# Kernel optimization log

Measured on AMD Instinct MI355X. Metric: run time of the kernel, lower is better.

The kernel has to match this reference:

```python
import jax, jax.numpy as jnp
import numpy as np

L_F, HOP, DELTA, L_S, COND, GH = 32, 16, 3, 96, 32, 64
B, T = 128, 48000


def setup_inputs() -> dict:
    key = jax.random.key(0)
    ks = jax.random.split(key, 12)
    s = 0.05
    return {
        "x": jax.random.normal(ks[0], (B, T), jnp.float32),
        # GRU (PyTorch layout): weight_ih (3H, L_S), weight_hh (3H, H)
        "W_ih": jax.random.normal(ks[1], (3 * GH, L_S), jnp.float32) * s,
        "W_hh": jax.random.normal(ks[2], (3 * GH, GH), jnp.float32) * s,
        "b_ih": jax.random.normal(ks[3], (3 * GH,), jnp.float32) * s,
        "b_hh": jax.random.normal(ks[4], (3 * GH,), jnp.float32) * s,
        # SlowBranch output projection -> cond_dim
        "W_cs": jax.random.normal(ks[5], (COND, GH), jnp.float32) * s,
        "b_cs": jax.random.normal(ks[6], (COND,), jnp.float32) * s,
        # FastEC MLP
        "W1": jax.random.normal(ks[7], (GH, L_F + COND), jnp.float32) * s,
        "b1": jax.random.normal(ks[8], (GH,), jnp.float32) * s,
        "W2": jax.random.normal(ks[9], (L_F, GH), jnp.float32) * s,
        "b2": jax.random.normal(ks[10], (L_F,), jnp.float32) * s,
    }


def reference(x, W_ih, W_hh, b_ih, b_hh, W_cs, b_cs, W1, b1, W2, b2):
    Bsz, Tlen = x.shape
    Nf = (Tlen - L_F) // HOP + 1
    win_s = DELTA * HOP * 2
    hop_s = DELTA * HOP
    Ns = (Tlen - win_s) // hop_s + 1

    f_starts = jnp.arange(Nf) * HOP                      # (Nf,)
    fast_idx = f_starts[:, None] + jnp.arange(L_F)       # (Nf, L_F)
    fast_frames = x[:, fast_idx]                         # (B, Nf, L_F)

    s_starts = jnp.arange(Ns) * hop_s
    slow_frames = x[:, s_starts[:, None] + jnp.arange(win_s)]  # (B, Ns, L_S)

    # Single-layer GRU over slow frames (PyTorch gate order r, z, n)
    def step(h, xt):
        gi = xt @ W_ih.T + b_ih                          # (B, 3H)
        gh = h @ W_hh.T + b_hh
        i_r, i_z, i_n = jnp.split(gi, 3, axis=-1)
        h_r, h_z, h_n = jnp.split(gh, 3, axis=-1)
        r = jax.nn.sigmoid(i_r + h_r)
        z = jax.nn.sigmoid(i_z + h_z)
        n = jnp.tanh(i_n + r * h_n)
        hn = (1.0 - z) * n + z * h
        return hn, hn

    h0 = jnp.zeros((Bsz, GH), x.dtype)
    _, hs = jax.lax.scan(step, h0, jnp.swapaxes(slow_frames, 0, 1))
    hs = jnp.swapaxes(hs, 0, 1)                          # (B, Ns, GH)
    c_s = hs @ W_cs.T + b_cs                             # (B, Ns, COND)

    # per-fast-frame conditioning vector (gather)
    idx = jnp.clip(jnp.arange(Nf) // DELTA - 1, 0, None)
    c = c_s[:, idx]                                      # (B, Nf, COND)

    # FastEC batched over all frames at once
    h = jnp.concatenate([fast_frames, c], axis=-1)       # (B, Nf, L_F+COND)
    h = jax.nn.relu(h @ W1.T + b1)
    y = h @ W2.T + b2                                    # (B, Nf, L_F)

    # overlap-add scatter
    out = jnp.zeros_like(x).at[:, fast_idx].add(y)
    return out
```

## Files before the change

kernel.cpp:

```cpp
#include <hip/hip_runtime.h>

constexpr int Bn  = 128;
constexpr int Tn  = 48000;
constexpr int NFn = 2999;
constexpr int NSn = 999;
constexpr int G3n = 192;
constexpr int GHn = 64;

typedef float f2 __attribute__((ext_vector_type(2)));

__global__ __launch_bounds__(192) void gi_kernel(const float* __restrict__ x,
                                                 const float* __restrict__ W_ih,
                                                 const float* __restrict__ b_ih,
                                                 float* __restrict__ GI) {
  __shared__ __align__(16) float WT[48 * 196];
  __shared__ float xs[1584];
  const int tile = blockIdx.x;
  const int b    = blockIdx.y;
  const int t0   = tile * 32;
  const int nt   = min(32, NSn - t0);
  const int tid  = threadIdx.x;

  const int span = (nt - 1) * 48 + 96;
  for (int i = tid; i < 1584; i += 192)
    xs[i] = (i < span) ? x[(size_t)b * Tn + t0 * 48 + i] : 0.0f;

  const int jq = tid % 48;
  const int tg = tid / 48;
  const int j0 = jq * 4;

  float acc[8][4];
#pragma unroll
  for (int u = 0; u < 8; ++u)
#pragma unroll
    for (int jj = 0; jj < 4; ++jj) acc[u][jj] = b_ih[j0 + jj];

  for (int half = 0; half < 2; ++half) {
    __syncthreads();
    for (int e = tid; e < 192 * 48; e += 192) {
      int j = e / 48, k = e % 48;
      WT[k * 196 + j] = W_ih[j * 96 + half * 48 + k];
    }
    __syncthreads();
    for (int k = 0; k < 48; ++k) {
      float4 w = *(const float4*)&WT[k * 196 + j0];
#pragma unroll
      for (int u = 0; u < 8; ++u) {
        float xv = xs[(tg * 8 + u) * 48 + half * 48 + k];
        acc[u][0] = fmaf(xv, w.x, acc[u][0]);
        acc[u][1] = fmaf(xv, w.y, acc[u][1]);
        acc[u][2] = fmaf(xv, w.z, acc[u][2]);
        acc[u][3] = fmaf(xv, w.w, acc[u][3]);
      }
    }
  }

#pragma unroll
  for (int u = 0; u < 8; ++u) {
    int tl = tg * 8 + u;
    if (tl < nt) {
      float4 st = make_float4(acc[u][0], acc[u][1], acc[u][2], acc[u][3]);
      *(float4*)&GI[(size_t)(b * NSn + t0 + tl) * G3n + j0] = st;
    }
  }
}

__device__ __forceinline__ float fsigmoid(float v) {
  return __fdividef(1.0f, 1.0f + __expf(-v));
}
__device__ __forceinline__ float ftanh_f(float v) {
  return 1.0f - __fdividef(2.0f, __expf(2.0f * v) + 1.0f);
}

__global__ __launch_bounds__(64, 1) void gru_kernel(const float* __restrict__ GI,
                                                    const float* __restrict__ W_hh,
                                                    const float* __restrict__ b_hh,
                                                    float* __restrict__ hs) {
  __shared__ __align__(16) float hbuf[64];
  const int b = blockIdx.x;
  const int j = threadIdx.x;

  f2 wr2[32], wz2[32], wn2[32];
  const f2* Wr = (const f2*)(W_hh + (size_t)j * 64);
  const f2* Wz = (const f2*)(W_hh + (size_t)(j + 64) * 64);
  const f2* Wn = (const f2*)(W_hh + (size_t)(j + 128) * 64);
#pragma unroll
  for (int q = 0; q < 32; ++q) { wr2[q] = Wr[q]; wz2[q] = Wz[q]; wn2[q] = Wn[q]; }
  const float br = b_hh[j], bz = b_hh[j + 64], bn = b_hh[j + 128];

  hbuf[j] = 0.0f;
  float hj = 0.0f;
  __syncthreads();

  const float* gp = GI + (size_t)b * NSn * G3n;
  float* hsp = hs + (size_t)b * NSn * GHn;

  float pr[3], pz[3], pn[3];
#pragma unroll
  for (int u = 0; u < 2; ++u) {
    pr[u] = gp[(size_t)u * G3n + j];
    pz[u] = gp[(size_t)u * G3n + 64 + j];
    pn[u] = gp[(size_t)u * G3n + 128 + j];
  }

  for (int t = 0; t < NSn; ++t) {
    const size_t off = (size_t)min(t + 2, NSn - 1) * G3n;
    pr[2] = gp[off + j];
    pz[2] = gp[off + 64 + j];
    pn[2] = gp[off + 128 + j];

    const f2* h2 = (const f2*)hbuf;
    f2 ar0 = {0.f, 0.f}, ar1 = {0.f, 0.f}, ar2 = {0.f, 0.f}, ar3 = {0.f, 0.f};
    f2 az0 = {0.f, 0.f}, az1 = {0.f, 0.f}, az2 = {0.f, 0.f}, az3 = {0.f, 0.f};
    f2 an0 = {0.f, 0.f}, an1 = {0.f, 0.f}, an2 = {0.f, 0.f}, an3 = {0.f, 0.f};
#pragma unroll
    for (int q = 0; q < 8; ++q) {
      f2 h0 = h2[q * 4 + 0], h1 = h2[q * 4 + 1], h2v = h2[q * 4 + 2], h3 = h2[q * 4 + 3];
      ar0 += wr2[q * 4 + 0] * h0; ar1 += wr2[q * 4 + 1] * h1;
      ar2 += wr2[q * 4 + 2] * h2v; ar3 += wr2[q * 4 + 3] * h3;
      az0 += wz2[q * 4 + 0] * h0; az1 += wz2[q * 4 + 1] * h1;
      az2 += wz2[q * 4 + 2] * h2v; az3 += wz2[q * 4 + 3] * h3;
      an0 += wn2[q * 4 + 0] * h0; an1 += wn2[q * 4 + 1] * h1;
      an2 += wn2[q * 4 + 2] * h2v; an3 += wn2[q * 4 + 3] * h3;
    }
    f2 sr = (ar0 + ar1) + (ar2 + ar3);
    f2 sz = (az0 + az1) + (az2 + az3);
    f2 sn = (an0 + an1) + (an2 + an3);

    float r = fsigmoid(pr[0] + br + sr.x + sr.y);
    float z = fsigmoid(pz[0] + bz + sz.x + sz.y);
    float n = ftanh_f(fmaf(r, bn + sn.x + sn.y, pn[0]));
    float hn = fmaf(z, hj - n, n);

    hbuf[j] = hn;
    hj = hn;
    hsp[(size_t)t * GHn + j] = hn;
    __syncthreads();

    pr[0] = pr[1]; pr[1] = pr[2];
    pz[0] = pz[1]; pz[1] = pz[2];
    pn[0] = pn[1]; pn[1] = pn[2];
  }
}

__global__ __launch_bounds__(256) void cs_kernel(const float* __restrict__ hs,
                                                 const float* __restrict__ W_cs,
                                                 const float* __restrict__ b_cs,
                                                 float* __restrict__ cs) {
  __shared__ __align__(16) float WcT[64 * 36];
  __shared__ __align__(16) float hsl[32 * 65];
  __shared__ __align__(16) float bcs[32];
  const int tile = blockIdx.x;
  const int b    = blockIdx.y;
  const int t0   = tile * 32;
  const int nt   = min(32, NSn - t0);
  const int tid  = threadIdx.x;

  for (int e = tid; e < 32 * 64; e += 256) {
    int i = e >> 6, k = e & 63;
    WcT[k * 36 + i] = W_cs[e];
  }
  for (int e = tid; e < nt * 64; e += 256) {
    int t = e >> 6, k = e & 63;
    hsl[t * 65 + k] = hs[((size_t)b * NSn + t0 + t) * GHn + k];
  }
  if (tid < 32) bcs[tid] = b_cs[tid];
  __syncthreads();

  const int oq = tid & 7;
  const int t  = tid >> 3;
  if (t < nt) {
    float4 acc = *(const float4*)&bcs[oq * 4];
    const float* hr = &hsl[t * 65];
#pragma unroll 4
    for (int k = 0; k < 64; ++k) {
      float hv = hr[k];
      float4 w = *(const float4*)&WcT[k * 36 + oq * 4];
      acc.x = fmaf(w.x, hv, acc.x);
      acc.y = fmaf(w.y, hv, acc.y);
      acc.z = fmaf(w.z, hv, acc.z);
      acc.w = fmaf(w.w, hv, acc.w);
    }
    *(float4*)&cs[((size_t)b * NSn + t0 + t) * 32 + oq * 4] = acc;
  }
}

__global__ __launch_bounds__(256) void out_kernel(const float* __restrict__ x,
                                                  const float* __restrict__ cs,
                                                  const float* __restrict__ W1,
                                                  const float* __restrict__ b1,
                                                  const float* __restrict__ W2,
                                                  const float* __restrict__ b2,
                                                  float* __restrict__ out) {
  __shared__ __align__(16) float A[33 * 65];
  __shared__ __align__(16) float W1T[64 * 68];
  __shared__ __align__(16) float W2T[64 * 36];
  __shared__ __align__(16) float h1loc[33 * 65];
  __shared__ __align__(16) float yloc[33 * 32];
  __shared__ __align__(16) float bb1[64];
  __shared__ __align__(16) float bb2[32];

  const int fb  = blockIdx.x;
  const int b   = blockIdx.y;
  const int f0  = fb * 32;
  const int nf  = min(33, NFn - f0);
  const int tid = threadIdx.x;

  for (int e = tid; e < 64 * 64; e += 256) {
    int o = e >> 6, k = e & 63;
    W1T[k * 68 + o] = W1[e];
  }
  for (int e = tid; e < 32 * 64; e += 256) {
    int o = e >> 6, k = e & 63;
    W2T[k * 36 + o] = W2[e];
  }
  if (tid < 64) bb1[tid] = b1[tid];
  if (tid < 32) bb2[tid] = b2[tid];

  for (int e = tid; e < 33 * 32; e += 256) {
    int lf = e >> 5, k = e & 31;
    int g = (f0 + lf) * 16 + k;
    A[lf * 65 + k] = (lf < nf && g < Tn) ? x[(size_t)b * Tn + g] : 0.0f;
  }
  for (int e = tid; e < 33 * 32; e += 256) {
    int lf = e >> 5, k = e & 31;
    int ts = max((f0 + lf) / 3 - 1, 0);
    A[lf * 65 + 32 + k] = (lf < nf) ? cs[((size_t)b * NSn + ts) * 32 + k] : 0.0f;
  }
  __syncthreads();

  for (int it = tid; it < 33 * 16; it += 256) {
    int lf = it >> 4, oq = it & 15;
    float4 acc = *(const float4*)&bb1[oq * 4];
    const float* ar = &A[lf * 65];
#pragma unroll 4
    for (int k = 0; k < 64; ++k) {
      float av = ar[k];
      float4 w = *(const float4*)&W1T[k * 68 + oq * 4];
      acc.x = fmaf(w.x, av, acc.x);
      acc.y = fmaf(w.y, av, acc.y);
      acc.z = fmaf(w.z, av, acc.z);
      acc.w = fmaf(w.w, av, acc.w);
    }
    acc.x = fmaxf(acc.x, 0.0f); acc.y = fmaxf(acc.y, 0.0f);
    acc.z = fmaxf(acc.z, 0.0f); acc.w = fmaxf(acc.w, 0.0f);
    *(float4*)&h1loc[lf * 65 + oq * 4] = acc;
  }
  __syncthreads();

  for (int it = tid; it < 33 * 8; it += 256) {
    int lf = it >> 3, oq = it & 7;
    float4 acc = *(const float4*)&bb2[oq * 4];
    const float* hr = &h1loc[lf * 65];
#pragma unroll 4
    for (int k = 0; k < 64; ++k) {
      float hv = hr[k];
      float4 w = *(const float4*)&W2T[k * 36 + oq * 4];
      acc.x = fmaf(w.x, hv, acc.x);
      acc.y = fmaf(w.y, hv, acc.y);
      acc.z = fmaf(w.z, hv, acc.z);
      acc.w = fmaf(w.w, hv, acc.w);
    }
    *(float4*)&yloc[lf * 32 + oq * 4] = acc;
  }
  __syncthreads();

  const int s0 = f0 * 16 + 16;
  const int s1 = min(s0 + 512, Tn);
  for (int s = s0 + tid; s < s1; s += 256) {
    int f1  = s >> 4;
    int o1  = s & 15;
    int lf1 = f1 - f0;
    float v = yloc[(lf1 - 1) * 32 + o1 + 16];
    if (lf1 < nf) v += yloc[lf1 * 32 + o1];
    out[(size_t)b * Tn + s] = v;
  }
  if (fb == 0 && tid < 16) out[(size_t)b * Tn + tid] = yloc[tid];
}

extern "C" void kernel_launch(void* const* d_in, const int* in_sizes, int n_in,
                              void* d_out, int out_size, void* d_ws, size_t ws_size,
                              hipStream_t stream) {
  const float* x    = (const float*)d_in[0];
  const float* W_ih = (const float*)d_in[1];
  const float* W_hh = (const float*)d_in[2];
  const float* b_ih = (const float*)d_in[3];
  const float* b_hh = (const float*)d_in[4];
  const float* W_cs = (const float*)d_in[5];
  const float* b_cs = (const float*)d_in[6];
  const float* W1   = (const float*)d_in[7];
  const float* b1   = (const float*)d_in[8];
  const float* W2   = (const float*)d_in[9];
  const float* b2   = (const float*)d_in[10];
  float* out = (float*)d_out;

  float* GI = (float*)d_ws;
  float* hs = GI + (size_t)Bn * NSn * G3n;
  float* cs = GI;

  gi_kernel<<<dim3(32, Bn), 192, 0, stream>>>(x, W_ih, b_ih, GI);
  gru_kernel<<<Bn, 64, 0, stream>>>(GI, W_hh, b_hh, hs);
  cs_kernel<<<dim3(32, Bn), 256, 0, stream>>>(hs, W_cs, b_cs, cs);
  out_kernel<<<dim3(94, Bn), 256, 0, stream>>>(x, cs, W1, b1, W2, b2, out);
}
```

Baseline: 888.9 us.

## Split GRU recurrence across 192 threads with chunked LDS staging of gates

The GRU kernel now uses 192 threads per batch element, with each thread computing one gate row of the W_hh·h product instead of three. Input gates for 32 timesteps are staged into LDS with vectorized loads, and hidden states are kept in LDS and written out in bulk per chunk. This shortens each thread's serial dot-product chain and replaces scattered per-step global loads and stores with coalesced ones. The cost is a second block barrier per timestep and an extra LDS round trip for the gate values.

New measurement: 887.4 us. Within noise of the previous version (-0.2%).

```diff
diff --git a/kernel.cpp b/kernel.cpp
--- a/kernel.cpp
+++ b/kernel.cpp
@@ -72,74 +72,75 @@
   return 1.0f - __fdividef(2.0f, __expf(2.0f * v) + 1.0f);
 }
 
-__global__ __launch_bounds__(64, 1) void gru_kernel(const float* __restrict__ GI,
-                                                    const float* __restrict__ W_hh,
-                                                    const float* __restrict__ b_hh,
-                                                    float* __restrict__ hs) {
-  __shared__ __align__(16) float hbuf[64];
-  const int b = blockIdx.x;
-  const int j = threadIdx.x;
-
-  f2 wr2[32], wz2[32], wn2[32];
-  const f2* Wr = (const f2*)(W_hh + (size_t)j * 64);
-  const f2* Wz = (const f2*)(W_hh + (size_t)(j + 64) * 64);
-  const f2* Wn = (const f2*)(W_hh + (size_t)(j + 128) * 64);
-#pragma unroll
-  for (int q = 0; q < 32; ++q) { wr2[q] = Wr[q]; wz2[q] = Wz[q]; wn2[q] = Wn[q]; }
-  const float br = b_hh[j], bz = b_hh[j + 64], bn = b_hh[j + 128];
-
-  hbuf[j] = 0.0f;
+__global__ __launch_bounds__(192, 1)
+void gru_kernel(const float* __restrict__ GI,
+                const float* __restrict__ W_hh,
+                const float* __restrict__ b_hh,
+                float* __restrict__ hs) {
+  __shared__ __align__(16) float gic[32 * 192];
+  __shared__ __align__(16) float hch[33 * 64];
+  __shared__ float gates[192];
+  const int b   = blockIdx.x;
+  const int tid = threadIdx.x;
+
+  f2 w[32];
+  const f2* Wp = (const f2*)(W_hh + (size_t)tid * 64);
+#pragma unroll
+  for (int q = 0; q < 32; ++q) w[q] = Wp[q];
+  const float bias = b_hh[tid];
+
+  if (tid < 64) hch[tid] = 0.0f;
   float hj = 0.0f;
-  __syncthreads();
-
-  const float* gp = GI + (size_t)b * NSn * G3n;
-  float* hsp = hs + (size_t)b * NSn * GHn;
-
-  float pr[3], pz[3], pn[3];
-#pragma unroll
-  for (int u = 0; u < 2; ++u) {
-    pr[u] = gp[(size_t)u * G3n + j];
-    pz[u] = gp[(size_t)u * G3n + 64 + j];
-    pn[u] = gp[(size_t)u * G3n + 128 + j];
-  }
-
-  for (int t = 0; t < NSn; ++t) {
-    const size_t off = (size_t)min(t + 2, NSn - 1) * G3n;
-    pr[2] = gp[off + j];
-    pz[2] = gp[off + 64 + j];
-    pn[2] = gp[off + 128 + j];
-
-    const f2* h2 = (const f2*)hbuf;
-    f2 ar0 = {0.f, 0.f}, ar1 = {0.f, 0.f}, ar2 = {0.f, 0.f}, ar3 = {0.f, 0.f};
-    f2 az0 = {0.f, 0.f}, az1 = {0.f, 0.f}, az2 = {0.f, 0.f}, az3 = {0.f, 0.f};
-    f2 an0 = {0.f, 0.f}, an1 = {0.f, 0.f}, an2 = {0.f, 0.f}, an3 = {0.f, 0.f};
-#pragma unroll
-    for (int q = 0; q < 8; ++q) {
-      f2 h0 = h2[q * 4 + 0], h1 = h2[q * 4 + 1], h2v = h2[q * 4 + 2], h3 = h2[q * 4 + 3];
-      ar0 += wr2[q * 4 + 0] * h0; ar1 += wr2[q * 4 + 1] * h1;
-      ar2 += wr2[q * 4 + 2] * h2v; ar3 += wr2[q * 4 + 3] * h3;
-      az0 += wz2[q * 4 + 0] * h0; az1 += wz2[q * 4 + 1] * h1;
-      az2 += wz2[q * 4 + 2] * h2v; az3 += wz2[q * 4 + 3] * h3;
-      an0 += wn2[q * 4 + 0] * h0; an1 += wn2[q * 4 + 1] * h1;
-      an2 += wn2[q * 4 + 2] * h2v; an3 += wn2[q * 4 + 3] * h3;
-    }
-    f2 sr = (ar0 + ar1) + (ar2 + ar3);
-    f2 sz = (az0 + az1) + (az2 + az3);
-    f2 sn = (an0 + an1) + (an2 + an3);
-
-    float r = fsigmoid(pr[0] + br + sr.x + sr.y);
-    float z = fsigmoid(pz[0] + bz + sz.x + sz.y);
-    float n = ftanh_f(fmaf(r, bn + sn.x + sn.y, pn[0]));
-    float hn = fmaf(z, hj - n, n);
-
-    hbuf[j] = hn;
-    hj = hn;
-    hsp[(size_t)t * GHn + j] = hn;
+
+  const float* gp  = GI + (size_t)b * NSn * G3n;
+  float* hsp       = hs + (size_t)b * NSn * GHn;
+
+  for (int t0 = 0; t0 < NSn; t0 += 32) {
+    const int nc = min(32, NSn - t0);
+
+    {
+      const float4* src = (const float4*)(gp + (size_t)t0 * G3n);
+      float4* dst = (float4*)gic;
+      for (int i = tid; i < nc * 48; i += 192) dst[i] = src[i];
+    }
     __syncthreads();
 
-    pr[0] = pr[1]; pr[1] = pr[2];
-    pz[0] = pz[1]; pz[1] = pz[2];
-    pn[0] = pn[1]; pn[1] = pn[2];
+    for (int c = 0; c < nc; ++c) {
+      const float4* h4 = (const float4*)&hch[c * 64];
+      f2 a0 = {0.f, 0.f}, a1 = {0.f, 0.f}, a2 = {0.f, 0.f}, a3 = {0.f, 0.f};
+#pragma unroll
+      for (int q = 0; q < 8; ++q) {
+        float4 hA = h4[2 * q];
+        float4 hB = h4[2 * q + 1];
+        a0 += w[4 * q + 0] * f2{hA.x, hA.y};
+        a1 += w[4 * q + 1] * f2{hA.z, hA.w};
+        a2 += w[4 * q + 2] * f2{hB.x, hB.y};
+        a3 += w[4 * q + 3] * f2{hB.z, hB.w};
+      }
+      f2 s = (a0 + a1) + (a2 + a3);
+      gates[tid] = bias + s.x + s.y;
+      __syncthreads();
+
+      if (tid < 64) {
+        float gr = gic[c * 192 + tid];
+        float gz = gic[c * 192 + 64 + tid];
+        float gn = gic[c * 192 + 128 + tid];
+        float r  = fsigmoid(gr + gates[tid]);
+        float z  = fsigmoid(gz + gates[tid + 64]);
+        float n  = ftanh_f(fmaf(r, gates[tid + 128], gn));
+        float hn = fmaf(z, hj - n, n);
+        hj = hn;
+        hch[(c + 1) * 64 + tid] = hn;
+      }
+      __syncthreads();
+    }
+
+    for (int i = tid; i < nc * 16; i += 192) {
+      int row = i >> 4, col = (i & 15) * 4;
+      *(float4*)&hsp[(size_t)(t0 + row) * GHn + col] =
+          *(const float4*)&hch[(row + 1) * 64 + col];
+    }
+    if (tid < 64) hch[tid] = hj;
   }
 }
 
@@ -299,7 +300,7 @@
   float* cs = GI;
 
   gi_kernel<<<dim3(32, Bn), 192, 0, stream>>>(x, W_ih, b_ih, GI);
-  gru_kernel<<<Bn, 64, 0, stream>>>(GI, W_hh, b_hh, hs);
+  gru_kernel<<<Bn, 192, 0, stream>>>(GI, W_hh, b_hh, hs);
   cs_kernel<<<dim3(32, Bn), 256, 0, stream>>>(hs, W_cs, b_cs, cs);
   out_kernel<<<dim3(94, Bn), 256, 0, stream>>>(x, cs, W1, b1, W2, b2, out);
 }
```
